# Performance work log

Hardware: AMD Instinct MI355X
Metric: run time of the kernel (lower is better)

## Reference

```python
import jax, jax.numpy as jnp
import numpy as np

N_HEADS = 12


def setup_inputs() -> dict:
    key = jax.random.key(0)
    ks = jax.random.split(key, 4)
    B, S, D = 2, 2048, 768
    x = jax.random.normal(ks[0], (B, S, D), dtype=jnp.float32)
    # nn.Linear-style init scale ~ 1/sqrt(D) to keep logits reasonable
    scale = 1.0 / np.sqrt(D)
    Wq = jax.random.normal(ks[1], (D, D), dtype=jnp.float32) * scale
    Wk = jax.random.normal(ks[2], (D, D), dtype=jnp.float32) * scale
    Wv = jax.random.normal(ks[3], (D, D), dtype=jnp.float32) * scale
    bq = jnp.zeros((D,), jnp.float32)
    bk = jnp.zeros((D,), jnp.float32)
    bv = jnp.zeros((D,), jnp.float32)
    mask = jnp.ones((B, S), jnp.int32)
    return {"x": x, "Wq": Wq, "bq": bq, "Wk": Wk, "bk": bk,
            "Wv": Wv, "bv": bv, "mask": mask}


def reference(x, Wq, bq, Wk, bk, Wv, bv, mask):
    B, S, D = x.shape
    H = N_HEADS
    W = D // H
    # q,k,v: (B,S,D) -> (B,H,S,W)
    def proj(Wm, bm):
        return (x @ Wm.T + bm).reshape(B, S, H, W).transpose(0, 2, 1, 3)
    q, k, v = proj(Wq, bq), proj(Wk, bk), proj(Wv, bv)
    scores = jnp.einsum("bhsw,bhtw->bhst", q, k) / jnp.sqrt(
        jnp.asarray(W, x.dtype))
    # mask: (B,S) -> broadcast over query positions; 0 -> -1e20
    scores = jnp.where(mask[:, None, None, :] == 0,
                       jnp.asarray(-1e20, scores.dtype), scores)
    attn = jax.nn.softmax(scores, axis=-1)  # (B,H,S,S)
    # dropout p=0.0 (eval) -> identity
    ctx = jnp.einsum("bhst,bhtw->bhsw", attn, v)
    hidden = ctx.transpose(0, 2, 1, 3).reshape(B, S, D)
    return hidden
```

## Files before the change

### kernel.cpp

```cpp
#include <hip/hip_runtime.h>
#include <hip/hip_bf16.h>
#include <stdint.h>


typedef __attribute__((ext_vector_type(8))) short bf16x8;
typedef __attribute__((ext_vector_type(4))) float f32x4;
typedef __attribute__((ext_vector_type(16))) float f32x16;
typedef __attribute__((ext_vector_type(8))) unsigned short u16x8;

#define MFMA16(a, b, c) __builtin_amdgcn_mfma_f32_16x16x32_bf16((a), (b), (c), 0, 0, 0)
#define MFMA32(a, b, c) __builtin_amdgcn_mfma_f32_32x32x16_bf16((a), (b), (c), 0, 0, 0)
#define SWZ(row, colb) ((colb) ^ (((row) & 7) << 4))

union U32x4BF {
  unsigned u[4];
  bf16x8 v;
};

__device__ __forceinline__ void gl_lds16(const void* g, void* l) {
  __builtin_amdgcn_global_load_lds(
      (__attribute__((address_space(1))) void*)const_cast<void*>(g),
      (__attribute__((address_space(3))) void*)l, 16, 0, 0);
}

__device__ __forceinline__ unsigned short f2bf(float x) {
  unsigned int v = __float_as_uint(x);
  return (unsigned short)((v + 0x7fffu + ((v >> 16) & 1u)) >> 16);
}

__global__ __launch_bounds__(256) void cvt_all(
    const float* __restrict__ x, const float* __restrict__ wq,
    const float* __restrict__ wk, const float* __restrict__ wv,
    unsigned short* __restrict__ xb, unsigned short* __restrict__ wb) {
  int i = blockIdx.x * 256 + threadIdx.x;
  const float* s;
  unsigned short* d;
  int off;
  if (i < 393216)      { s = x;  d = xb;            off = i; }
  else if (i < 466944) { s = wq; d = wb;            off = i - 393216; }
  else if (i < 540672) { s = wk; d = wb + 589824;   off = i - 466944; }
  else                 { s = wv; d = wb + 1179648;  off = i - 540672; }
  const float4* sp = (const float4*)s + (size_t)off * 2;
  float4 a = sp[0], b2 = sp[1];
  u16x8 o;
  o[0] = f2bf(a.x); o[1] = f2bf(a.y); o[2] = f2bf(a.z); o[3] = f2bf(a.w);
  o[4] = f2bf(b2.x); o[5] = f2bf(b2.y); o[6] = f2bf(b2.z); o[7] = f2bf(b2.w);
  *((u16x8*)d + off) = o;
}

__global__ __launch_bounds__(256) void proj_gemm(
    const unsigned short* __restrict__ xb, const unsigned short* __restrict__ wb,
    const float* __restrict__ bq, const float* __restrict__ bk, const float* __restrict__ bv,
    unsigned short* __restrict__ qw, unsigned short* __restrict__ kw,
    unsigned short* __restrict__ vw) {
  __shared__ __align__(16) char psmem[49152];
  const int t = threadIdx.x, lane = t & 63, wave = t >> 6;
  const int lo = lane & 15, hi = lane >> 4;
  const int wr = wave >> 1, wc = wave & 1;
  const int mbase = blockIdx.x * 128;
  const int wsel = blockIdx.y / 6;
  const int nbase = (blockIdx.y % 6) * 128;
  const char* xc = (const char*)xb;
  const char* wmc = (const char*)(wb + (size_t)wsel * 589824);

  const int pp0 = t * 16, pp1 = t * 16 + 4096;
  const int ar0 = pp0 >> 7, ac0 = (pp0 & 127) ^ ((ar0 & 7) << 4);
  const int am0 = ((ac0 >> 6) << 6) + ar0, ak0 = ac0 & 63;
  const int ar1 = pp1 >> 7, ac1 = (pp1 & 127) ^ ((ar1 & 7) << 4);
  const int am1 = ((ac1 >> 6) << 6) + ar1, ak1 = ac1 & 63;

  const char* xa0 = xc + (size_t)(mbase + am0) * 1536 + ak0;
  const char* xa1 = xc + (size_t)(mbase + am1) * 1536 + ak1;
  const char* wa0 = wmc + (size_t)(nbase + am0) * 1536 + ak0;
  const char* wa1 = wmc + (size_t)(nbase + am1) * 1536 + ak1;

#define PSTAGE(BUF)                              \
  do {                                           \
    char* lb = psmem + (BUF) * 16384;            \
    gl_lds16(xa0, lb + pp0);                     \
    gl_lds16(xa1, lb + pp1);                     \
    gl_lds16(wa0, lb + 8192 + pp0);              \
    gl_lds16(wa1, lb + 8192 + pp1);              \
    xa0 += 64; xa1 += 64; wa0 += 64; wa1 += 64;  \
  } while (0)

  f32x4 acc[4][4];
#pragma unroll
  for (int i = 0; i < 4; i++)
#pragma unroll
    for (int j = 0; j < 4; j++) acc[i][j] = (f32x4){0.f, 0.f, 0.f, 0.f};

  const int axor = (lo & 7) << 4;
  PSTAGE(0);
  PSTAGE(1);
  int cur = 0, sb = 2;
#pragma unroll 1
  for (int it = 0; it < 24; ++it) {
    if (it < 22) {
      PSTAGE(sb);
      asm volatile("s_waitcnt vmcnt(8)" ::: "memory");
    } else if (it == 22) {
      asm volatile("s_waitcnt vmcnt(4)" ::: "memory");
    } else {
      asm volatile("s_waitcnt vmcnt(0)" ::: "memory");
    }
    __builtin_amdgcn_s_barrier();
    const char* lA = psmem + cur * 16384;
    const char* lB = lA + 8192;

    bf16x8 af[4], bf[4];
#pragma unroll
    for (int mf = 0; mf < 4; mf++)
      af[mf] = *(const bf16x8*)(lA + (mf * 16 + lo) * 128 + ((wr * 64 + hi * 16) ^ axor));
#pragma unroll
    for (int nf = 0; nf < 4; nf++)
      bf[nf] = *(const bf16x8*)(lB + (nf * 16 + lo) * 128 + ((wc * 64 + hi * 16) ^ axor));

    __builtin_amdgcn_s_setprio(1);
    if (wsel == 2) {
#pragma unroll
      for (int mf = 0; mf < 4; mf++)
#pragma unroll
        for (int nf = 0; nf < 4; nf++) acc[mf][nf] = MFMA16(bf[nf], af[mf], acc[mf][nf]);
    } else {
#pragma unroll
      for (int mf = 0; mf < 4; mf++)
#pragma unroll
        for (int nf = 0; nf < 4; nf++) acc[mf][nf] = MFMA16(af[mf], bf[nf], acc[mf][nf]);
    }
    __builtin_amdgcn_s_setprio(0);
    __builtin_amdgcn_s_barrier();
    cur = (cur == 2) ? 0 : cur + 1;
    sb = (sb == 2) ? 0 : sb + 1;
  }
#undef PSTAGE

  const float QSCALE = 0.125f * 1.44269504089f;
  if (wsel == 2) {
#pragma unroll
    for (int nf = 0; nf < 4; nf++) {
#pragma unroll
      for (int mf = 0; mf < 4; mf++) {
#pragma unroll
        for (int r = 0; r < 4; r++) {
          int n = nbase + wc * 64 + nf * 16 + hi * 4 + r;
          int m = mbase + wr * 64 + mf * 16 + lo;
          int b_ = m >> 11, s = m & 2047;
          int h = n >> 6, wcol = n & 63;
          float val = acc[mf][nf][r] + bv[n];
          vw[(((size_t)b_ * 12 + h) * 64 + wcol) * 2048 + s] = f2bf(val);
        }
      }
    }
  } else {
    const float* bias = (wsel == 0) ? bq : bk;
#pragma unroll
    for (int nf = 0; nf < 4; nf++) {
      int n = nbase + wc * 64 + nf * 16 + lo;
      float bv_ = bias[n];
      int h = n >> 6, wcol = n & 63;
#pragma unroll
      for (int mf = 0; mf < 4; mf++) {
#pragma unroll
        for (int r = 0; r < 4; r++) {
          int m = mbase + wr * 64 + mf * 16 + hi * 4 + r;
          int b_ = m >> 11, s = m & 2047;
          float val = acc[mf][nf][r] + bv_;
          size_t bhh = (size_t)b_ * 12 + h;
          if (wsel == 0)
            qw[(bhh * 2048 + s) * 64 + wcol] = f2bf(val * QSCALE);
          else
            kw[(bhh * 2048 + s) * 64 + wcol] = f2bf(val);
        }
      }
    }
  }
}

__global__ __launch_bounds__(256) void attn_kernel(
    const unsigned short* __restrict__ qw, const unsigned short* __restrict__ kw,
    const unsigned short* __restrict__ vw, const int* __restrict__ mask,
    float* __restrict__ out) {
  __shared__ __align__(16) char smem[49664];
  const int t = threadIdx.x, lane = t & 63, wave = t >> 6;
  const int wq = wave >> 1, wk = wave & 1;
  const int l31 = lane & 31, hl = lane >> 5;
  const int qb = blockIdx.x, bh = blockIdx.y;
  const int b = bh / 12, hh = bh - b * 12;

  {
    const int* mb = mask + (size_t)b * 2048 + t * 8;
    int4 a0 = *(const int4*)mb;
    int4 a1 = *(const int4*)(mb + 4);
    unsigned by = (unsigned)(a0.x != 0) | ((unsigned)(a0.y != 0) << 1) |
                  ((unsigned)(a0.z != 0) << 2) | ((unsigned)(a0.w != 0) << 3) |
                  ((unsigned)(a1.x != 0) << 4) | ((unsigned)(a1.y != 0) << 5) |
                  ((unsigned)(a1.z != 0) << 6) | ((unsigned)(a1.w != 0) << 7);
    smem[49152 + t] = (char)by;
  }
  asm volatile("s_waitcnt lgkmcnt(0)" ::: "memory");

  bf16x8 qv[4];
  {
    int qrow = qb * 64 + wq * 32 + l31;
    const char* qp = (const char*)qw + ((size_t)bh * 2048 + qrow) * 128 + hl * 16;
#pragma unroll
    for (int s = 0; s < 4; s++) qv[s] = *(const bf16x8*)(qp + s * 32);
  }

  const int p0 = t * 16, p1 = t * 16 + 4096;
  const int r0 = p0 >> 9, c0 = (p0 >> 7) & 3, o0 = (p0 & 127) ^ ((r0 & 7) << 4);
  const int r1 = p1 >> 9, c1 = (p1 >> 7) & 3, o1 = (p1 & 127) ^ ((r1 & 7) << 4);

  const char* kp0 = (const char*)kw + (size_t)bh * 262144 + (c0 * 16 + r0) * 128 + o0;
  const char* kp1 = (const char*)kw + (size_t)bh * 262144 + (c1 * 16 + r1) * 128 + o1;
  const char* vp0 = (const char*)vw + (size_t)bh * 262144 + (size_t)(c0 * 16 + r0) * 4096 + o0;
  const char* vp1 = (const char*)vw + (size_t)bh * 262144 + (size_t)(c1 * 16 + r1) * 4096 + o1;

#define STAGEP(BUF_)                              \
  do {                                            \
    char* kb_ = smem + (BUF_) * 16384;            \
    gl_lds16(kp0, kb_ + p0);                      \
    gl_lds16(kp1, kb_ + p1);                      \
    gl_lds16(vp0, kb_ + 8192 + p0);               \
    gl_lds16(vp1, kb_ + 8192 + p1);               \
    kp0 += 8192; kp1 += 8192; vp0 += 128; vp1 += 128; \
  } while (0)

  f32x16 oacc[2], lsacc;
#pragma unroll
  for (int wh = 0; wh < 2; wh++)
#pragma unroll
    for (int g = 0; g < 16; g++) oacc[wh][g] = 0.f;
#pragma unroll
  for (int g = 0; g < 16; g++) lsacc[g] = 0.f;
  U32x4BF onesv;
  onesv.u[0] = onesv.u[1] = onesv.u[2] = onesv.u[3] = 0x3F803F80u;

  const int kbl = (l31 & 15) * 512 + (wk * 2 + (l31 >> 4)) * 128;
  const int rxor = (l31 & 7) << 4;
  const int hl16 = hl * 16;

  STAGEP(0);
  STAGEP(1);

#define BODY(IT_, BUF_, DOSTAGE_, SBUF_, VMW_)                                         \
  {                                                                                    \
    if (DOSTAGE_) STAGEP(SBUF_);                                                       \
    asm volatile("s_waitcnt vmcnt(" #VMW_ ")" ::: "memory");                           \
    __builtin_amdgcn_s_barrier();                                                      \
    const char* lKc_ = smem + (BUF_) * 16384;                                          \
    const char* lVc_ = lKc_ + 8192;                                                    \
    f32x16 sc_;                                                                        \
    _Pragma("unroll") for (int g = 0; g < 16; g++) sc_[g] = 0.f;                       \
    __builtin_amdgcn_s_setprio(1);                                                     \
    _Pragma("unroll") for (int s = 0; s < 4; s++) {                                    \
      bf16x8 kf_ = *(const bf16x8*)(lKc_ + kbl + ((s * 32 + hl16) ^ rxor));            \
      sc_ = MFMA32(kf_, qv[s], sc_);                                                   \
    }                                                                                  \
    __builtin_amdgcn_s_setprio(0);                                                     \
    unsigned long long bal_ = *(const unsigned long long*)(smem + 49152 + (IT_) * 8);  \
    if (bal_ != ~0ull) {                                                               \
      _Pragma("unroll") for (int g = 0; g < 16; g++) {                                 \
        int key_ = wk * 32 + 4 * hl + (g & 3) + 8 * (g >> 2);                          \
        if (!((bal_ >> key_) & 1)) sc_[g] = -30000.f;                                  \
      }                                                                                \
    }                                                                                  \
    float e_[16];                                                                      \
    _Pragma("unroll") for (int g = 0; g < 16; g++)                                     \
        asm("v_exp_f32 %0, %1" : "=v"(e_[g]) : "v"(sc_[g]));                           \
    unsigned pk_[4][2];                                                                \
    _Pragma("unroll") for (int m = 0; m < 4; m++) {                                    \
      asm("v_cvt_pk_bf16_f32 %0, %1, %2"                                               \
          : "=v"(pk_[m][0]) : "v"(e_[4 * m]), "v"(e_[4 * m + 1]));                     \
      asm("v_cvt_pk_bf16_f32 %0, %1, %2"                                               \
          : "=v"(pk_[m][1]) : "v"(e_[4 * m + 2]), "v"(e_[4 * m + 3]));                 \
    }                                                                                  \
    U32x4BF apv_[2];                                                                   \
    _Pragma("unroll") for (int sp = 0; sp < 2; sp++)                                   \
        _Pragma("unroll") for (int cp = 0; cp < 2; cp++) {                             \
      unsigned xx_ = pk_[2 * sp][cp], yy_ = pk_[2 * sp + 1][cp];                       \
      asm("v_permlane32_swap_b32 %0, %1" : "+v"(xx_), "+v"(yy_));                      \
      apv_[sp].u[cp] = xx_;                                                            \
      apv_[sp].u[2 + cp] = yy_;                                                        \
    }                                                                                  \
    __builtin_amdgcn_s_setprio(1);                                                     \
    lsacc = MFMA32(apv_[0].v, onesv.v, lsacc);                                         \
    lsacc = MFMA32(apv_[1].v, onesv.v, lsacc);                                         \
    _Pragma("unroll") for (int wh = 0; wh < 2; wh++) {                                 \
      int vbl_ = (l31 & 15) * 512 + (wh * 2 + (l31 >> 4)) * 128;                       \
      _Pragma("unroll") for (int sp = 0; sp < 2; sp++) {                               \
        bf16x8 vf_ =                                                                   \
            *(const bf16x8*)(lVc_ + vbl_ + ((wk * 64 + sp * 32 + hl16) ^ rxor));       \
        oacc[wh] = MFMA32(apv_[sp].v, vf_, oacc[wh]);                                  \
      }                                                                                \
    }                                                                                  \
    __builtin_amdgcn_s_setprio(0);                                                     \
    __builtin_amdgcn_s_barrier();         \
  }

#pragma unroll 1
  for (int itb = 0; itb < 30; itb += 3) {
    BODY(itb, 0, 1, 2, 8);
    BODY(itb + 1, 1, 1, 0, 8);
    BODY(itb + 2, 2, 1, 1, 8);
  }
  BODY(30, 0, 0, 0, 4);
  BODY(31, 1, 0, 0, 0);
#undef BODY
#undef STAGEP

  if (wk == 1) {
    if (l31 == 0) {
#pragma unroll
      for (int g = 0; g < 16; g++) {
        int qrow = 4 * hl + (g & 3) + 8 * (g >> 2);
        *(float*)(smem + 49408 + (wq * 32 + qrow) * 4) = lsacc[g];
      }
    }
#pragma unroll
    for (int wh = 0; wh < 2; wh++) {
      int vrow = wh * 32 + l31;
#pragma unroll
      for (int m = 0; m < 4; m++) {
        f32x4 part = (f32x4){oacc[wh][4 * m], oacc[wh][4 * m + 1],
                             oacc[wh][4 * m + 2], oacc[wh][4 * m + 3]};
        *(f32x4*)(smem + wq * 8192 + vrow * 128 + SWZ(vrow, hl * 16 + m * 32)) = part;
      }
    }
  }
  __syncthreads();
  if (wk == 0) {
    float linv[16];
#pragma unroll
    for (int g = 0; g < 16; g++) {
      int qrow = 4 * hl + (g & 3) + 8 * (g >> 2);
      float l1 = *(const float*)(smem + 49408 + (wq * 32 + qrow) * 4);
      linv[g] = __builtin_amdgcn_rcpf(lsacc[g] + l1);
    }
#pragma unroll
    for (int wh = 0; wh < 2; wh++) {
      int vrow = wh * 32 + l31;
#pragma unroll
      for (int m = 0; m < 4; m++) {
        f32x4 part = *(const f32x4*)(smem + wq * 8192 + vrow * 128 + SWZ(vrow, hl * 16 + m * 32));
#pragma unroll
        for (int r = 0; r < 4; r++) {
          int g = 4 * m + r;
          int qrow = 4 * hl + r + 8 * m;
          float val = (oacc[wh][g] + part[r]) * linv[g];
          out[((size_t)b * 2048 + qb * 64 + wq * 32 + qrow) * 768 + hh * 64 + wh * 32 + l31] =
              val;
        }
      }
    }
  }
}

extern "C" void kernel_launch(void* const* d_in, const int* in_sizes, int n_in,
                              void* d_out, int out_size, void* d_ws, size_t ws_size,
                              hipStream_t stream) {
  (void)in_sizes; (void)n_in; (void)out_size; (void)ws_size;
  const float* x  = (const float*)d_in[0];
  const float* Wq = (const float*)d_in[1];
  const float* bq = (const float*)d_in[2];
  const float* Wk = (const float*)d_in[3];
  const float* bk = (const float*)d_in[4];
  const float* Wv = (const float*)d_in[5];
  const float* bv = (const float*)d_in[6];
  const int* mask = (const int*)d_in[7];
  float* out = (float*)d_out;

  char* ws = (char*)d_ws;
  unsigned short* xb = (unsigned short*)(ws);
  unsigned short* wb = (unsigned short*)(ws + 6291456);
  unsigned short* qw = (unsigned short*)(ws + 9830400);
  unsigned short* kw = (unsigned short*)(ws + 16121856);
  unsigned short* vw = (unsigned short*)(ws + 22413312);

  cvt_all<<<2400, 256, 0, stream>>>(x, Wq, Wk, Wv, xb, wb);
  proj_gemm<<<dim3(32, 18), 256, 0, stream>>>(xb, wb, bq, bk, bv, qw, kw, vw);
  attn_kernel<<<dim3(32, 24), 256, 0, stream>>>(qw, kw, vw, mask, out);
}
```

Measured before the change: 84.25 us.

## Load V fragments directly to registers and deepen K LDS ring

```diff
diff --git a/kernel.cpp b/kernel.cpp
--- a/kernel.cpp
+++ b/kernel.cpp
@@ -177,11 +177,11 @@
   }
 }
 
-__global__ __launch_bounds__(256) void attn_kernel(
+__global__ __launch_bounds__(256, 4) void attn_kernel(
     const unsigned short* __restrict__ qw, const unsigned short* __restrict__ kw,
     const unsigned short* __restrict__ vw, const int* __restrict__ mask,
     float* __restrict__ out) {
-  __shared__ __align__(16) char smem[49664];
+  __shared__ __align__(16) char smem[33280];
   const int t = threadIdx.x, lane = t & 63, wave = t >> 6;
   const int wq = wave >> 1, wk = wave & 1;
   const int l31 = lane & 31, hl = lane >> 5;
@@ -196,9 +196,8 @@
                   ((unsigned)(a0.z != 0) << 2) | ((unsigned)(a0.w != 0) << 3) |
                   ((unsigned)(a1.x != 0) << 4) | ((unsigned)(a1.y != 0) << 5) |
                   ((unsigned)(a1.z != 0) << 6) | ((unsigned)(a1.w != 0) << 7);
-    smem[49152 + t] = (char)by;
-  }
-  asm volatile("s_waitcnt lgkmcnt(0)" ::: "memory");
+    smem[32768 + t] = (char)by;
+  }
 
   bf16x8 qv[4];
   {
@@ -211,20 +210,19 @@
   const int p0 = t * 16, p1 = t * 16 + 4096;
   const int r0 = p0 >> 9, c0 = (p0 >> 7) & 3, o0 = (p0 & 127) ^ ((r0 & 7) << 4);
   const int r1 = p1 >> 9, c1 = (p1 >> 7) & 3, o1 = (p1 & 127) ^ ((r1 & 7) << 4);
-
   const char* kp0 = (const char*)kw + (size_t)bh * 262144 + (c0 * 16 + r0) * 128 + o0;
   const char* kp1 = (const char*)kw + (size_t)bh * 262144 + (c1 * 16 + r1) * 128 + o1;
-  const char* vp0 = (const char*)vw + (size_t)bh * 262144 + (size_t)(c0 * 16 + r0) * 4096 + o0;
-  const char* vp1 = (const char*)vw + (size_t)bh * 262144 + (size_t)(c1 * 16 + r1) * 4096 + o1;
-
-#define STAGEP(BUF_)                              \
-  do {                                            \
-    char* kb_ = smem + (BUF_) * 16384;            \
-    gl_lds16(kp0, kb_ + p0);                      \
-    gl_lds16(kp1, kb_ + p1);                      \
-    gl_lds16(vp0, kb_ + 8192 + p0);               \
-    gl_lds16(vp1, kb_ + 8192 + p1);               \
-    kp0 += 8192; kp1 += 8192; vp0 += 128; vp1 += 128; \
+
+  const char* vptr0 = (const char*)vw + (size_t)bh * 262144 + (size_t)l31 * 4096 +
+                      wk * 64 + hl * 16;
+  const char* vptr1 = vptr0 + (size_t)32 * 4096;
+
+#define STAGEP(BUF_)                       \
+  do {                                     \
+    char* kb_ = smem + (BUF_) * 8192;      \
+    gl_lds16(kp0, kb_ + p0);               \
+    gl_lds16(kp1, kb_ + p1);               \
+    kp0 += 8192; kp1 += 8192;              \
   } while (0)
 
   f32x16 oacc[2], lsacc;
@@ -241,16 +239,23 @@
   const int rxor = (l31 & 7) << 4;
   const int hl16 = hl * 16;
 
+  asm volatile("s_waitcnt lgkmcnt(0)" ::: "memory");
   STAGEP(0);
   STAGEP(1);
-
-#define BODY(IT_, BUF_, DOSTAGE_, SBUF_, VMW_)                                         \
+  __syncthreads();
+
+#define BODY(IT_, BUF_, DOSTAGE_, SBUF_, VMTOP_, VMPV_)                                \
   {                                                                                    \
+    bf16x8 vf00 = *(const bf16x8*)(vptr0);                                             \
+    bf16x8 vf01 = *(const bf16x8*)(vptr0 + 32);                                        \
+    bf16x8 vf10 = *(const bf16x8*)(vptr1);                                             \
+    bf16x8 vf11 = *(const bf16x8*)(vptr1 + 32);                                        \
+    vptr0 += 128; vptr1 += 128;                                                        \
+    asm volatile("" ::: "memory");           \
     if (DOSTAGE_) STAGEP(SBUF_);                                                       \
-    asm volatile("s_waitcnt vmcnt(" #VMW_ ")" ::: "memory");                           \
+    asm volatile("s_waitcnt vmcnt(" #VMTOP_ ")" ::: "memory");                         \
     __builtin_amdgcn_s_barrier();                                                      \
-    const char* lKc_ = smem + (BUF_) * 16384;                                          \
-    const char* lVc_ = lKc_ + 8192;                                                    \
+    const char* lKc_ = smem + (BUF_) * 8192;                                           \
     f32x16 sc_;                                                                        \
     _Pragma("unroll") for (int g = 0; g < 16; g++) sc_[g] = 0.f;                       \
     __builtin_amdgcn_s_setprio(1);                                                     \
@@ -259,7 +264,7 @@
       sc_ = MFMA32(kf_, qv[s], sc_);                                                   \
     }                                                                                  \
     __builtin_amdgcn_s_setprio(0);                                                     \
-    unsigned long long bal_ = *(const unsigned long long*)(smem + 49152 + (IT_) * 8);  \
+    unsigned long long bal_ = *(const unsigned long long*)(smem + 32768 + (IT_) * 8);  \
     if (bal_ != ~0ull) {                                                               \
       _Pragma("unroll") for (int g = 0; g < 16; g++) {                                 \
         int key_ = wk * 32 + 4 * hl + (g & 3) + 8 * (g >> 2);                          \
@@ -287,35 +292,38 @@
     __builtin_amdgcn_s_setprio(1);                                                     \
     lsacc = MFMA32(apv_[0].v, onesv.v, lsacc);                                         \
     lsacc = MFMA32(apv_[1].v, onesv.v, lsacc);                                         \
-    _Pragma("unroll") for (int wh = 0; wh < 2; wh++) {                                 \
-      int vbl_ = (l31 & 15) * 512 + (wh * 2 + (l31 >> 4)) * 128;                       \
-      _Pragma("unroll") for (int sp = 0; sp < 2; sp++) {                               \
-        bf16x8 vf_ =                                                                   \
-            *(const bf16x8*)(lVc_ + vbl_ + ((wk * 64 + sp * 32 + hl16) ^ rxor));       \
-        oacc[wh] = MFMA32(apv_[sp].v, vf_, oacc[wh]);                                  \
-      }                                                                                \
-    }                                                                                  \
     __builtin_amdgcn_s_setprio(0);                                                     \
-    __builtin_amdgcn_s_barrier();         \
+    asm volatile("s_waitcnt vmcnt(" #VMPV_ ")" ::: "memory");                          \
+    __builtin_amdgcn_s_setprio(1);                                                     \
+    oacc[0] = MFMA32(apv_[0].v, vf00, oacc[0]);                                        \
+    oacc[0] = MFMA32(apv_[1].v, vf01, oacc[0]);                                        \
+    oacc[1] = MFMA32(apv_[0].v, vf10, oacc[1]);                                        \
+    oacc[1] = MFMA32(apv_[1].v, vf11, oacc[1]);                                        \
+    __builtin_amdgcn_s_setprio(0);                                                     \
   }
 
 #pragma unroll 1
-  for (int itb = 0; itb < 30; itb += 3) {
-    BODY(itb, 0, 1, 2, 8);
-    BODY(itb + 1, 1, 1, 0, 8);
-    BODY(itb + 2, 2, 1, 1, 8);
-  }
-  BODY(30, 0, 0, 0, 4);
-  BODY(31, 1, 0, 0, 0);
+  for (int itb = 0; itb < 28; itb += 4) {
+    BODY(itb, 0, 1, 2, 8, 2);
+    BODY(itb + 1, 1, 1, 3, 8, 2);
+    BODY(itb + 2, 2, 1, 0, 8, 2);
+    BODY(itb + 3, 3, 1, 1, 8, 2);
+  }
+  BODY(28, 0, 1, 2, 8, 2);
+  BODY(29, 1, 1, 3, 8, 2);
+  BODY(30, 2, 1, 0, 8, 2);
+  BODY(31, 3, 0, 0, 6, 0);
 #undef BODY
 #undef STAGEP
 
+  __syncthreads();
+
   if (wk == 1) {
     if (l31 == 0) {
 #pragma unroll
       for (int g = 0; g < 16; g++) {
         int qrow = 4 * hl + (g & 3) + 8 * (g >> 2);
-        *(float*)(smem + 49408 + (wq * 32 + qrow) * 4) = lsacc[g];
+        *(float*)(smem + 33024 + (wq * 32 + qrow) * 4) = lsacc[g];
       }
     }
 #pragma unroll
@@ -335,7 +343,7 @@
 #pragma unroll
     for (int g = 0; g < 16; g++) {
       int qrow = 4 * hl + (g & 3) + 8 * (g >> 2);
-      float l1 = *(const float*)(smem + 49408 + (wq * 32 + qrow) * 4);
+      float l1 = *(const float*)(smem + 33024 + (wq * 32 + qrow) * 4);
       linv[g] = __builtin_amdgcn_rcpf(lsacc[g] + l1);
     }
 #pragma unroll
```

Measured after the change: 147.3 us. +74.8%, slower.

## Software-pipeline QK^T of the next tile with softmax and PV of the previous

Applied to the files above, without the earlier changes.

```diff
diff --git a/kernel.cpp b/kernel.cpp
--- a/kernel.cpp
+++ b/kernel.cpp
@@ -198,7 +198,6 @@
                   ((unsigned)(a1.z != 0) << 6) | ((unsigned)(a1.w != 0) << 7);
     smem[49152 + t] = (char)by;
   }
-  asm volatile("s_waitcnt lgkmcnt(0)" ::: "memory");
 
   bf16x8 qv[4];
   {
@@ -217,17 +216,17 @@
   const char* vp0 = (const char*)vw + (size_t)bh * 262144 + (size_t)(c0 * 16 + r0) * 4096 + o0;
   const char* vp1 = (const char*)vw + (size_t)bh * 262144 + (size_t)(c1 * 16 + r1) * 4096 + o1;
 
-#define STAGEP(BUF_)                              \
-  do {                                            \
-    char* kb_ = smem + (BUF_) * 16384;            \
-    gl_lds16(kp0, kb_ + p0);                      \
-    gl_lds16(kp1, kb_ + p1);                      \
-    gl_lds16(vp0, kb_ + 8192 + p0);               \
-    gl_lds16(vp1, kb_ + 8192 + p1);               \
+#define STAGEP(BUF_)                                  \
+  do {                                                \
+    char* kb_ = smem + (BUF_) * 16384;                \
+    gl_lds16(kp0, kb_ + p0);                          \
+    gl_lds16(kp1, kb_ + p1);                          \
+    gl_lds16(vp0, kb_ + 8192 + p0);                   \
+    gl_lds16(vp1, kb_ + 8192 + p1);                   \
     kp0 += 8192; kp1 += 8192; vp0 += 128; vp1 += 128; \
   } while (0)
 
-  f32x16 oacc[2], lsacc;
+  f32x16 oacc[2], lsacc, scA, scB;
 #pragma unroll
   for (int wh = 0; wh < 2; wh++)
 #pragma unroll
@@ -241,73 +240,94 @@
   const int rxor = (l31 & 7) << 4;
   const int hl16 = hl * 16;
 
+#define SMPV(ITP_, BPV_, SCP_)                                                          \
+  {                                                                                     \
+    unsigned long long bal_ = *(const unsigned long long*)(smem + 49152 + (ITP_) * 8);  \
+    if (bal_ != ~0ull) {                                                                \
+      _Pragma("unroll") for (int g = 0; g < 16; g++) {                                  \
+        int key_ = wk * 32 + 4 * hl + (g & 3) + 8 * (g >> 2);                           \
+        if (!((bal_ >> key_) & 1)) SCP_[g] = -30000.f;                                  \
+      }                                                                                 \
+    }                                                                                   \
+    _Pragma("unroll") for (int g = 0; g < 16; g++) {                                    \
+      float t_;                                                                         \
+      asm("v_exp_f32 %0, %1" : "=v"(t_) : "v"(SCP_[g]));                                \
+      SCP_[g] = t_;                                                                     \
+    }                                                                                   \
+    unsigned pk_[4][2];                                                                 \
+    _Pragma("unroll") for (int m = 0; m < 4; m++) {                                     \
+      asm("v_cvt_pk_bf16_f32 %0, %1, %2"                                                \
+          : "=v"(pk_[m][0]) : "v"(SCP_[4 * m]), "v"(SCP_[4 * m + 1]));                  \
+      asm("v_cvt_pk_bf16_f32 %0, %1, %2"                                                \
+          : "=v"(pk_[m][1]) : "v"(SCP_[4 * m + 2]), "v"(SCP_[4 * m + 3]));              \
+    }                                                                                   \
+    U32x4BF apv_[2];                                                                    \
+    _Pragma("unroll") for (int sp = 0; sp < 2; sp++)                                    \
+        _Pragma("unroll") for (int cp = 0; cp < 2; cp++) {                              \
+      unsigned xx_ = pk_[2 * sp][cp], yy_ = pk_[2 * sp + 1][cp];                        \
+      asm("v_permlane32_swap_b32 %0, %1" : "+v"(xx_), "+v"(yy_));                       \
+      apv_[sp].u[cp] = xx_;                                                             \
+      apv_[sp].u[2 + cp] = yy_;                                                         \
+    }                                                                                   \
+    __builtin_amdgcn_s_setprio(1);                                                      \
+    lsacc = MFMA32(apv_[0].v, onesv.v, lsacc);                                          \
+    lsacc = MFMA32(apv_[1].v, onesv.v, lsacc);                                          \
+    const char* lVc_ = smem + (BPV_) * 16384 + 8192;                                    \
+    _Pragma("unroll") for (int wh = 0; wh < 2; wh++) {                                  \
+      int vbl_ = (l31 & 15) * 512 + (wh * 2 + (l31 >> 4)) * 128;                        \
+      _Pragma("unroll") for (int sp = 0; sp < 2; sp++) {                                \
+        bf16x8 vf_ = *(const bf16x8*)(lVc_ + vbl_ + ((wk * 64 + sp * 32 + hl16) ^ rxor)); \
+        oacc[wh] = MFMA32(apv_[sp].v, vf_, oacc[wh]);                                   \
+      }                                                                                 \
+    }                                                                                   \
+    __builtin_amdgcn_s_setprio(0);                                                      \
+  }
+
+#define BODY(IT_, BQK_, SBUF_, BPV_, DOSTG_, VMW_, SCQ_, SCP_)                \
+  {                                                                           \
+    if (DOSTG_) STAGEP(SBUF_);                                                \
+    asm volatile("s_waitcnt vmcnt(" #VMW_ ")" ::: "memory");                  \
+    __builtin_amdgcn_s_barrier();                                             \
+    const char* lKc_ = smem + (BQK_) * 16384;                                 \
+    _Pragma("unroll") for (int g = 0; g < 16; g++) SCQ_[g] = 0.f;             \
+    __builtin_amdgcn_s_setprio(1);                                            \
+    _Pragma("unroll") for (int s = 0; s < 4; s++) {                           \
+      bf16x8 kf_ = *(const bf16x8*)(lKc_ + kbl + ((s * 32 + hl16) ^ rxor));   \
+      SCQ_ = MFMA32(kf_, qv[s], SCQ_);                                        \
+    }                                                                         \
+    __builtin_amdgcn_s_setprio(0);                                            \
+    SMPV((IT_) - 1, BPV_, SCP_);                                              \
+    __builtin_amdgcn_s_barrier();                                             \
+  }
+
   STAGEP(0);
   STAGEP(1);
-
-#define BODY(IT_, BUF_, DOSTAGE_, SBUF_, VMW_)                                         \
-  {                                                                                    \
-    if (DOSTAGE_) STAGEP(SBUF_);                                                       \
-    asm volatile("s_waitcnt vmcnt(" #VMW_ ")" ::: "memory");                           \
-    __builtin_amdgcn_s_barrier();                                                      \
-    const char* lKc_ = smem + (BUF_) * 16384;                                          \
-    const char* lVc_ = lKc_ + 8192;                                                    \
-    f32x16 sc_;                                                                        \
-    _Pragma("unroll") for (int g = 0; g < 16; g++) sc_[g] = 0.f;                       \
-    __builtin_amdgcn_s_setprio(1);                                                     \
-    _Pragma("unroll") for (int s = 0; s < 4; s++) {                                    \
-      bf16x8 kf_ = *(const bf16x8*)(lKc_ + kbl + ((s * 32 + hl16) ^ rxor));            \
-      sc_ = MFMA32(kf_, qv[s], sc_);                                                   \
-    }                                                                                  \
-    __builtin_amdgcn_s_setprio(0);                                                     \
-    unsigned long long bal_ = *(const unsigned long long*)(smem + 49152 + (IT_) * 8);  \
-    if (bal_ != ~0ull) {                                                               \
-      _Pragma("unroll") for (int g = 0; g < 16; g++) {                                 \
-        int key_ = wk * 32 + 4 * hl + (g & 3) + 8 * (g >> 2);                          \
-        if (!((bal_ >> key_) & 1)) sc_[g] = -30000.f;                                  \
-      }                                                                                \
-    }                                                                                  \
-    float e_[16];                                                                      \
-    _Pragma("unroll") for (int g = 0; g < 16; g++)                                     \
-        asm("v_exp_f32 %0, %1" : "=v"(e_[g]) : "v"(sc_[g]));                           \
-    unsigned pk_[4][2];                                                                \
-    _Pragma("unroll") for (int m = 0; m < 4; m++) {                                    \
-      asm("v_cvt_pk_bf16_f32 %0, %1, %2"                                               \
-          : "=v"(pk_[m][0]) : "v"(e_[4 * m]), "v"(e_[4 * m + 1]));                     \
-      asm("v_cvt_pk_bf16_f32 %0, %1, %2"                                               \
-          : "=v"(pk_[m][1]) : "v"(e_[4 * m + 2]), "v"(e_[4 * m + 3]));                 \
-    }                                                                                  \
-    U32x4BF apv_[2];                                                                   \
-    _Pragma("unroll") for (int sp = 0; sp < 2; sp++)                                   \
-        _Pragma("unroll") for (int cp = 0; cp < 2; cp++) {                             \
-      unsigned xx_ = pk_[2 * sp][cp], yy_ = pk_[2 * sp + 1][cp];                       \
-      asm("v_permlane32_swap_b32 %0, %1" : "+v"(xx_), "+v"(yy_));                      \
-      apv_[sp].u[cp] = xx_;                                                            \
-      apv_[sp].u[2 + cp] = yy_;                                                        \
-    }                                                                                  \
-    __builtin_amdgcn_s_setprio(1);                                                     \
-    lsacc = MFMA32(apv_[0].v, onesv.v, lsacc);                                         \
-    lsacc = MFMA32(apv_[1].v, onesv.v, lsacc);                                         \
-    _Pragma("unroll") for (int wh = 0; wh < 2; wh++) {                                 \
-      int vbl_ = (l31 & 15) * 512 + (wh * 2 + (l31 >> 4)) * 128;                       \
-      _Pragma("unroll") for (int sp = 0; sp < 2; sp++) {                               \
-        bf16x8 vf_ =                                                                   \
-            *(const bf16x8*)(lVc_ + vbl_ + ((wk * 64 + sp * 32 + hl16) ^ rxor));       \
-        oacc[wh] = MFMA32(apv_[sp].v, vf_, oacc[wh]);                                  \
-      }                                                                                \
-    }                                                                                  \
-    __builtin_amdgcn_s_setprio(0);                                                     \
-    __builtin_amdgcn_s_barrier();         \
+  asm volatile("s_waitcnt vmcnt(4) lgkmcnt(0)" ::: "memory");
+  __builtin_amdgcn_s_barrier();
+  {
+    const char* lKc_ = smem;
+#pragma unroll
+    for (int g = 0; g < 16; g++) scA[g] = 0.f;
+#pragma unroll
+    for (int s = 0; s < 4; s++) {
+      bf16x8 kf_ = *(const bf16x8*)(lKc_ + kbl + ((s * 32 + hl16) ^ rxor));
+      scA = MFMA32(kf_, qv[s], scA);
+    }
   }
 
 #pragma unroll 1
-  for (int itb = 0; itb < 30; itb += 3) {
-    BODY(itb, 0, 1, 2, 8);
-    BODY(itb + 1, 1, 1, 0, 8);
-    BODY(itb + 2, 2, 1, 1, 8);
-  }
-  BODY(30, 0, 0, 0, 4);
-  BODY(31, 1, 0, 0, 0);
+  for (int itb = 1; itb < 31; itb += 6) {
+    BODY(itb + 0, 1, 2, 0, 1, 4, scB, scA);
+    BODY(itb + 1, 2, 0, 1, 1, 4, scA, scB);
+    BODY(itb + 2, 0, 1, 2, 1, 4, scB, scA);
+    BODY(itb + 3, 1, 2, 0, 1, 4, scA, scB);
+    BODY(itb + 4, 2, 0, 1, 1, 4, scB, scA);
+    BODY(itb + 5, 0, 1, 2, 1, 4, scA, scB);
+  }
+  BODY(31, 1, 0, 0, 0, 0, scB, scA);
+  SMPV(31, 1, scB);
 #undef BODY
+#undef SMPV
 #undef STAGEP
 
   if (wk == 1) {
```

Result: faster. 82.52 us (-2.1%).
